# Optimization experiments

Measured on AMD Instinct MI355X. Metric: run time of the kernel, lower is better.

The kernel has to match this reference:

```python
import jax, jax.numpy as jnp
import numpy as np

N = 33554432  # 2**25 flattened (strike x maturity) grid points


def setup_inputs() -> dict:
    key = jax.random.key(0)
    k1, k2 = jax.random.split(key)
    logm = 0.3 * jax.random.normal(k1, (N,), dtype=jnp.float32)
    # yATM (ATM total variance) must be > 0; map U[0,1) -> [0.02, 0.5]
    yATM = 0.02 + 0.48 * jax.random.uniform(k2, (N,), dtype=jnp.float32)
    return {
        "logm": logm,
        "yATM": yATM,
        "raw_rho": jnp.array([0.5], dtype=jnp.float32),
        "raw_eta": jnp.array([0.0], dtype=jnp.float32),
        "raw_gamma": jnp.array([0.0], dtype=jnp.float32),
    }


def _ssvi_out(logm, yATM, raw_rho, raw_eta, raw_gamma):
    rho = jnp.tanh(raw_rho)            # scalar-ish [1], broadcasts
    eta = jnp.exp(raw_eta)
    gamma = jnp.exp(raw_gamma)
    # power-law phi: eta / (y^gamma * (1+y)^(1-gamma))
    phi = eta / (jnp.power(yATM, gamma) * jnp.power(1.0 + yATM, 1.0 - gamma))
    pl = phi * logm
    return yATM * 0.5 * (1.0 + rho * pl + jnp.sqrt(pl * pl + 2.0 * rho * pl + 1.0))


def reference(logm, yATM, raw_rho, raw_eta, raw_gamma):
    out_fn = lambda lm: _ssvi_out(lm, yATM, raw_rho, raw_eta, raw_gamma)
    output = out_fn(logm)
    sum_out = lambda lm: jnp.sum(out_fn(lm))
    grad_logm1 = jax.grad(sum_out)(logm)                      # d(sum out)/d logm (elementwise)
    grad_logm2 = jax.grad(lambda lm: jnp.sum(jax.grad(sum_out)(lm)))(logm)
    grad_ttm1 = jnp.zeros_like(logm)
    return (output, grad_ttm1, grad_logm1, grad_logm2)
```

## Files before the change

kernel.cpp:

```cpp
#include <hip/hip_runtime.h>
#include <math.h>


__global__ __launch_bounds__(256) void ssvi_kernel(
    const float4* __restrict__ logm4,
    const float4* __restrict__ y4,
    const float* __restrict__ raw_rho,
    const float* __restrict__ raw_eta,
    const float* __restrict__ raw_gamma,
    float4* __restrict__ out4,
    int n4)
{
    int i = blockIdx.x * blockDim.x + threadIdx.x;
    if (i >= n4) return;

    const float rho   = tanhf(raw_rho[0]);
    const float eta   = expf(raw_eta[0]);
    const float gamma = expf(raw_gamma[0]);
    const float one_m_rho2 = 1.0f - rho * rho;

    float4 lm = logm4[i];
    float4 yv = y4[i];

    float4 o, g1, g2;
    const float* lmp = &lm.x;
    const float* yp  = &yv.x;
    float* op  = &o.x;
    float* g1p = &g1.x;
    float* g2p = &g2.x;

    #pragma unroll
    for (int k = 0; k < 4; ++k) {
        float y  = yp[k];
        float l  = lmp[k];
        float phi = eta / (powf(y, gamma) * powf(1.0f + y, 1.0f - gamma));
        float pl  = phi * l;
        float s2  = pl * pl + 2.0f * rho * pl + 1.0f;
        float s   = sqrtf(s2);
        float inv_s = 1.0f / s;
        float half_y = 0.5f * y;
        op[k]  = half_y * (1.0f + rho * pl + s);
        g1p[k] = half_y * phi * (rho + (pl + rho) * inv_s);
        g2p[k] = half_y * phi * phi * one_m_rho2 * (inv_s * inv_s * inv_s);
    }

    out4[i] = o;
    out4[(size_t)n4 + i] = make_float4(0.0f, 0.0f, 0.0f, 0.0f);
    out4[2 * (size_t)n4 + i] = g1;
    out4[3 * (size_t)n4 + i] = g2;
}

extern "C" void kernel_launch(void* const* d_in, const int* in_sizes, int n_in,
                              void* d_out, int out_size, void* d_ws, size_t ws_size,
                              hipStream_t stream) {
    const float4* logm4 = (const float4*)d_in[0];
    const float4* y4    = (const float4*)d_in[1];
    const float* raw_rho   = (const float*)d_in[2];
    const float* raw_eta   = (const float*)d_in[3];
    const float* raw_gamma = (const float*)d_in[4];
    float4* out4 = (float4*)d_out;

    int n  = in_sizes[0];
    int n4 = n / 4;
    int block = 256;
    int grid = (n4 + block - 1) / block;
    ssvi_kernel<<<grid, block, 0, stream>>>(logm4, y4, raw_rho, raw_eta, raw_gamma,
                                            out4, n4);
}
```

Before: 828.8 us.

## Use hardware exp2/log2/rsq intrinsics, nontemporal memory ops, two vectors per thread

Replaces powf, the division and sqrtf with native log2/exp2/rsq intrinsics, folding the two powers into a single exp2 of a blended log. Loads and stores now use nontemporal hints, and each thread handles two float4 chunks with the grid halved. This is meant to remove the heavy transcendental instruction cost and cache pollution on a streaming kernel. In exchange, the native intrinsics have slightly lower accuracy and denormal handling than the library calls.

```diff
diff --git a/kernel.cpp b/kernel.cpp
--- a/kernel.cpp
+++ b/kernel.cpp
@@ -2,68 +2,89 @@
 #include <math.h>
 
 
+typedef float f32x4 __attribute__((ext_vector_type(4)));
+
+__device__ __forceinline__ float ex2(float x) { return __builtin_amdgcn_exp2f(x); }
+__device__ __forceinline__ float lg2(float x) { return __builtin_amdgcn_logf(x); }
+__device__ __forceinline__ float rsq(float x) { return __builtin_amdgcn_rsqf(x); }
+
+#define LOG2E 1.4426950408889634f
+
 __global__ __launch_bounds__(256) void ssvi_kernel(
-    const float4* __restrict__ logm4,
-    const float4* __restrict__ y4,
+    const f32x4* __restrict__ logm4,
+    const f32x4* __restrict__ y4,
     const float* __restrict__ raw_rho,
     const float* __restrict__ raw_eta,
     const float* __restrict__ raw_gamma,
-    float4* __restrict__ out4,
+    f32x4* __restrict__ out4,
     int n4)
 {
-    int i = blockIdx.x * blockDim.x + threadIdx.x;
-    if (i >= n4) return;
+    const float rr   = raw_rho[0];
+    const float e2t  = ex2(2.0f * LOG2E * rr);
+    const float rho  = (e2t - 1.0f) * __builtin_amdgcn_rcpf(e2t + 1.0f);
+    const float eta  = ex2(LOG2E * raw_eta[0]);
+    const float gamma = ex2(LOG2E * raw_gamma[0]);
+    const float omr2 = 1.0f - rho * rho;
+    const float two_rho = rho + rho;
 
-    const float rho   = tanhf(raw_rho[0]);
-    const float eta   = expf(raw_eta[0]);
-    const float gamma = expf(raw_gamma[0]);
-    const float one_m_rho2 = 1.0f - rho * rho;
-
-    float4 lm = logm4[i];
-    float4 yv = y4[i];
-
-    float4 o, g1, g2;
-    const float* lmp = &lm.x;
-    const float* yp  = &yv.x;
-    float* op  = &o.x;
-    float* g1p = &g1.x;
-    float* g2p = &g2.x;
+    const int base = blockIdx.x * (256 * 2) + threadIdx.x;
+    const f32x4 zero4 = {0.0f, 0.0f, 0.0f, 0.0f};
 
     #pragma unroll
-    for (int k = 0; k < 4; ++k) {
-        float y  = yp[k];
-        float l  = lmp[k];
-        float phi = eta / (powf(y, gamma) * powf(1.0f + y, 1.0f - gamma));
-        float pl  = phi * l;
-        float s2  = pl * pl + 2.0f * rho * pl + 1.0f;
-        float s   = sqrtf(s2);
-        float inv_s = 1.0f / s;
-        float half_y = 0.5f * y;
-        op[k]  = half_y * (1.0f + rho * pl + s);
-        g1p[k] = half_y * phi * (rho + (pl + rho) * inv_s);
-        g2p[k] = half_y * phi * phi * one_m_rho2 * (inv_s * inv_s * inv_s);
+    for (int j = 0; j < 2; ++j) {
+        const int idx = base + j * 256;
+        if (idx >= n4) continue;
+
+        f32x4 lm = __builtin_nontemporal_load(&logm4[idx]);
+        f32x4 yv = __builtin_nontemporal_load(&y4[idx]);
+
+        f32x4 o, g1, g2;
+
+        #pragma unroll
+        for (int k = 0; k < 4; ++k) {
+            float y = yv[k];
+            float l = lm[k];
+
+            float l2y  = lg2(y);
+            float yp1  = 1.0f + y;
+            float l2y1 = lg2(yp1);
+            float t    = fmaf(gamma, l2y - l2y1, l2y1);
+            float phi  = eta * ex2(-t);
+
+            float pl  = phi * l;
+            float s2  = fmaf(pl, pl, fmaf(two_rho, pl, 1.0f));
+            float is  = rsq(s2);
+            float s   = s2 * is;
+            float hy  = 0.5f * y;
+            float hphi = hy * phi;
+            float is3 = (is * is) * is;
+
+            o[k]  = hy * (fmaf(rho, pl, 1.0f) + s);
+            g1[k] = hphi * fmaf(pl + rho, is, rho);
+            g2[k] = (hphi * phi) * (omr2 * is3);
+        }
+
+        __builtin_nontemporal_store(o,     &out4[idx]);
+        __builtin_nontemporal_store(zero4, &out4[(size_t)n4 + idx]);
+        __builtin_nontemporal_store(g1,    &out4[2 * (size_t)n4 + idx]);
+        __builtin_nontemporal_store(g2,    &out4[3 * (size_t)n4 + idx]);
     }
-
-    out4[i] = o;
-    out4[(size_t)n4 + i] = make_float4(0.0f, 0.0f, 0.0f, 0.0f);
-    out4[2 * (size_t)n4 + i] = g1;
-    out4[3 * (size_t)n4 + i] = g2;
 }
 
 extern "C" void kernel_launch(void* const* d_in, const int* in_sizes, int n_in,
                               void* d_out, int out_size, void* d_ws, size_t ws_size,
                               hipStream_t stream) {
-    const float4* logm4 = (const float4*)d_in[0];
-    const float4* y4    = (const float4*)d_in[1];
+    const f32x4* logm4 = (const f32x4*)d_in[0];
+    const f32x4* y4    = (const f32x4*)d_in[1];
     const float* raw_rho   = (const float*)d_in[2];
     const float* raw_eta   = (const float*)d_in[3];
     const float* raw_gamma = (const float*)d_in[4];
-    float4* out4 = (float4*)d_out;
+    f32x4* out4 = (f32x4*)d_out;
 
     int n  = in_sizes[0];
     int n4 = n / 4;
     int block = 256;
-    int grid = (n4 + block - 1) / block;
+    int grid = (n4 + block * 2 - 1) / (block * 2);
     ssvi_kernel<<<grid, block, 0, stream>>>(logm4, y4, raw_rho, raw_eta, raw_gamma,
                                             out4, n4);
 }
```

Result: faster. 689.3 us (-16.8%).
